# Optimization experiments

Hardware: AMD Instinct MI355X
Metric: run time of the kernel (lower is better)

The kernel has to match this reference:

```python
import jax, jax.numpy as jnp
import numpy as np

SIZES = [384, 160, 128, 96, 1]   # aev_length followed by hidden sizes (ANI-1 config)
N_SPECIES = 4                    # H, C, N, O
N_LAYERS = 4
CELU_ALPHA = 0.1
B, A = 128, 512                  # molecules, atoms per molecule


def setup_inputs() -> dict:
    key = jax.random.key(0)
    ks = jax.random.split(key, 2 + 2 * N_LAYERS)
    inp = {
        "fullaev": jax.random.normal(ks[0], (B, A, SIZES[0]), dtype=jnp.float32),
        "species": jax.random.randint(ks[1], (A,), 0, N_SPECIES, dtype=jnp.int32),
    }
    # Per-species stacked Linear params, torch default init: U(-1/sqrt(fan_in), 1/sqrt(fan_in))
    for l in range(N_LAYERS):
        bound = 1.0 / np.sqrt(SIZES[l])
        inp[f"W{l}"] = jax.random.uniform(ks[2 + 2 * l], (N_SPECIES, SIZES[l + 1], SIZES[l]),
                                          dtype=jnp.float32, minval=-bound, maxval=bound)
        inp[f"b{l}"] = jax.random.uniform(ks[3 + 2 * l], (N_SPECIES, SIZES[l + 1]),
                                          dtype=jnp.float32, minval=-bound, maxval=bound)
    return inp


def reference(fullaev, species, W0, b0, W1, b1, W2, b2, W3, b3):
    # fullaev: [B, A, aev_len]; species: [A] int route ids.
    # Equivalent to the per-atom Python loop: each atom goes through its
    # species' MLP; gather the per-atom weight matrices and do one batched GEMM per layer.
    Ws = (W0, W1, W2, W3)
    bs = (b0, b1, b2, b3)
    y = fullaev
    for l in range(N_LAYERS):
        Wa = Ws[l][species]          # [A, out, in] gathered per atom
        ba = bs[l][species]          # [A, out]
        y = jnp.einsum('bai,aoi->bao', y, Wa) + ba[None, :, :]
        if l < N_LAYERS - 1:
            y = jax.nn.celu(y, alpha=CELU_ALPHA)
    # stack over atoms + sum reducer over atom dim, then squeeze -> [B]
    return jnp.squeeze(jnp.sum(y, axis=1), axis=-1)
```

## Files before the change

kernel.cpp:

```cpp
#include <hip/hip_runtime.h>
#include <hip/hip_bf16.h>


typedef float f32x4 __attribute__((ext_vector_type(4)));
typedef short s16x8 __attribute__((ext_vector_type(8)));

#define NMOL   128
#define NATOM  512
#define AEV    384
#define MT     64
#define Y0LD   168
#define Y1LD   136
#define Y2LD   104

#define PL0    61440
#define PL1    20480
#define PL2    12288
#define BASE0  0
#define BASE1  245760
#define BASE2  327680
#define WP_BYTE_OFF 262144

typedef const __attribute__((address_space(1))) void* gas_ptr;
typedef __attribute__((address_space(3))) void* las_ptr;

__device__ __forceinline__ ushort f2bf(float f) {
    uint u = __float_as_uint(f);
    return (ushort)((u + 0x7fffu + ((u >> 16) & 1u)) >> 16);
}
__device__ __forceinline__ float bf2f(ushort h) {
    return __uint_as_float(((uint)h) << 16);
}
__device__ __forceinline__ float celu_f(float v) {
    return fmaxf(v, 0.0f) + fminf(0.1f * (__expf(10.0f * v) - 1.0f), 0.0f);
}
__device__ __forceinline__ uint pk2bf(float x, float y) {
    __hip_bfloat162 h2;
    h2.x = __float2bfloat16(x);
    h2.y = __float2bfloat16(y);
    return *(uint*)&h2;
}

__global__ __launch_bounds__(256) void prep_kernel(
    const float* __restrict__ W0, const float* __restrict__ W1,
    const float* __restrict__ W2, ushort* __restrict__ Wp)
{
    const int idx = blockIdx.x * 256 + threadIdx.x;
    int n, k0, KS;
    size_t base;
    const float* src;
    if (idx < 30720) {
        const int s = idx / 7680, r = idx % 7680;
        n = r / 48; k0 = (r % 48) * 8; KS = 12;
        src = W0 + (size_t)idx * 8;
        base = BASE0 + (size_t)s * PL0;
    } else if (idx < 40960) {
        const int i2 = idx - 30720;
        const int s = i2 / 2560, r = i2 % 2560;
        n = r / 20; k0 = (r % 20) * 8; KS = 5;
        src = W1 + (size_t)i2 * 8;
        base = BASE1 + (size_t)s * PL1;
    } else {
        const int i2 = idx - 40960;
        const int s = i2 / 1536, r = i2 % 1536;
        n = r / 16; k0 = (r % 16) * 8; KS = 4;
        src = W2 + (size_t)i2 * 8;
        base = BASE2 + (size_t)s * PL2;
    }
    const float4 v0 = *(const float4*)(src);
    const float4 v1 = *(const float4*)(src + 4);
    const size_t fo = (size_t)((((n >> 4) * KS + (k0 >> 5)) * 64
                                + ((k0 & 31) >> 3) * 16 + (n & 15)) * 8);
    uint4 w;
    w.x = (uint)f2bf(v0.x) | ((uint)f2bf(v0.y) << 16);
    w.y = (uint)f2bf(v0.z) | ((uint)f2bf(v0.w) << 16);
    w.z = (uint)f2bf(v1.x) | ((uint)f2bf(v1.y) << 16);
    w.w = (uint)f2bf(v1.z) | ((uint)f2bf(v1.w) << 16);
    *(uint4*)(Wp + base + fo) = w;
}

__global__ __attribute__((amdgpu_flat_work_group_size(512, 512),
                          amdgpu_waves_per_eu(8, 8)))
void ani_mfma_kernel(
    const float* __restrict__ aev, const int* __restrict__ species,
    const ushort* __restrict__ Wp,
    const float* __restrict__ b0, const float* __restrict__ b1,
    const float* __restrict__ b2,
    const float* __restrict__ W3, const float* __restrict__ b3,
    float* __restrict__ partial)
{
    __shared__ __align__(16) unsigned char smemA[17408];
    __shared__ __align__(16) unsigned char smemB[21504];

    const int bid  = blockIdx.x;
    const int a    = bid >> 1;
    const int half = bid & 1;
    const int tid  = threadIdx.x;
    const int lane = tid & 63;
    const int wid  = tid >> 6;
    const int mgrp = wid >> 2;
    const int ngrp = wid & 3;
    const bool has3 = (ngrp < 2);

    const int s = species[a];
    const ushort* Bh0 = Wp + BASE0 + (size_t)s * PL0;
    const ushort* Bh1 = Wp + BASE1 + (size_t)s * PL1;
    const ushort* Bh2 = Wp + BASE2 + (size_t)s * PL2;
    const float* b0s = b0 + s * 160;
    const float* b1s = b1 + s * 128;
    const float* b2s = b2 + s * 96;
    const float* w3s = W3 + s * 96;
    const float  bb3 = b3[s];

    ushort* y0buf = (ushort*)smemB;
    ushort* y1buf = (ushort*)smemA;

    const int mol8 = lane >> 3;
    const int swz  = (lane & 7) ^ mol8;
    const char* gsrc = (const char*)(aev
        + ((size_t)(half * MT + wid * 8 + mol8) * NATOM + a) * AEV) + swz * 16;
    const int ldsbase = wid * 1024;

    const f32x4 zero = {0.f, 0.f, 0.f, 0.f};
    f32x4 acc[2][3];
    #pragma unroll
    for (int mf = 0; mf < 2; ++mf)
        #pragma unroll
        for (int ti = 0; ti < 3; ++ti) acc[mf][ti] = zero;

    {
        const int r0 = mgrp * 32 + (lane & 15);
        const int c  = lane >> 4;

        __builtin_amdgcn_global_load_lds((gas_ptr)(gsrc),
                                         (las_ptr)(smemA + ldsbase), 16, 0, 0);
        __syncthreads();

        #pragma unroll
        for (int t = 0; t < 12; ++t) {
            if (t < 11)
                __builtin_amdgcn_global_load_lds(
                    (gas_ptr)(gsrc + (t + 1) * 128),
                    (las_ptr)(smemA + (((t + 1) & 1) * 8192) + ldsbase), 16, 0, 0);

            const float* Xb = (const float*)(smemA + (t & 1) * 8192);
            s16x8 ah[2];
            #pragma unroll
            for (int mf = 0; mf < 2; ++mf) {
                const int r = r0 + mf * 16;
                const float* rowp = Xb + r * 32;
                const f32x4 c0 = *(const f32x4*)(rowp + (((2 * c    ) ^ (r & 7)) * 4));
                const f32x4 c1 = *(const f32x4*)(rowp + (((2 * c + 1) ^ (r & 7)) * 4));
                union { s16x8 v; uint u[4]; } rr;
                rr.u[0] = pk2bf(c0.x, c0.y);
                rr.u[1] = pk2bf(c0.z, c0.w);
                rr.u[2] = pk2bf(c1.x, c1.y);
                rr.u[3] = pk2bf(c1.z, c1.w);
                ah[mf] = rr.v;
            }
            #pragma unroll
            for (int ti = 0; ti < 3; ++ti) {
                if (ti < 2 || has3) {
                    const s16x8 bh = *(const s16x8*)(
                        Bh0 + ((size_t)((ngrp + 4 * ti) * 12 + t) * 64 + lane) * 8);
                    acc[0][ti] = __builtin_amdgcn_mfma_f32_16x16x32_bf16(ah[0], bh, acc[0][ti], 0, 0, 0);
                    acc[1][ti] = __builtin_amdgcn_mfma_f32_16x16x32_bf16(ah[1], bh, acc[1][ti], 0, 0, 0);
                }
            }
            if (t < 11) __syncthreads();
        }
    }

    s16x8 b1r[2][5];
    #pragma unroll
    for (int ks = 0; ks < 5; ++ks) {
        b1r[0][ks] = *(const s16x8*)(Bh1 + ((size_t)((ngrp    ) * 5 + ks) * 64 + lane) * 8);
        b1r[1][ks] = *(const s16x8*)(Bh1 + ((size_t)((ngrp + 4) * 5 + ks) * 64 + lane) * 8);
    }

    #pragma unroll
    for (int ti = 0; ti < 3; ++ti) {
        if (ti < 2 || has3) {
            const int n = (ngrp + 4 * ti) * 16 + (lane & 15);
            const float bv = b0s[n];
            #pragma unroll
            for (int mf = 0; mf < 2; ++mf) {
                #pragma unroll
                for (int r = 0; r < 4; ++r) {
                    const int row = mgrp * 32 + mf * 16 + (lane >> 4) * 4 + r;
                    y0buf[row * Y0LD + n] = f2bf(celu_f(acc[mf][ti][r] + bv));
                }
            }
        }
    }
    __syncthreads();

    f32x4 acc1[2][2];
    #pragma unroll
    for (int mf = 0; mf < 2; ++mf) { acc1[mf][0] = zero; acc1[mf][1] = zero; }
    #pragma unroll
    for (int ks = 0; ks < 5; ++ks) {
        s16x8 ah[2];
        #pragma unroll
        for (int mf = 0; mf < 2; ++mf)
            ah[mf] = *(const s16x8*)(y0buf + (mgrp * 32 + mf * 16 + (lane & 15)) * Y0LD
                                     + ks * 32 + (lane >> 4) * 8);
        #pragma unroll
        for (int mf = 0; mf < 2; ++mf) {
            acc1[mf][0] = __builtin_amdgcn_mfma_f32_16x16x32_bf16(ah[mf], b1r[0][ks], acc1[mf][0], 0, 0, 0);
            acc1[mf][1] = __builtin_amdgcn_mfma_f32_16x16x32_bf16(ah[mf], b1r[1][ks], acc1[mf][1], 0, 0, 0);
        }
    }

    s16x8 b2r[2][4];
    #pragma unroll
    for (int ks = 0; ks < 4; ++ks)
        b2r[0][ks] = *(const s16x8*)(Bh2 + ((size_t)((ngrp) * 4 + ks) * 64 + lane) * 8);
    if (has3) {
        #pragma unroll
        for (int ks = 0; ks < 4; ++ks)
            b2r[1][ks] = *(const s16x8*)(Bh2 + ((size_t)((ngrp + 4) * 4 + ks) * 64 + lane) * 8);
    }

    #pragma unroll
    for (int t = 0; t < 2; ++t) {
        const int n = (ngrp + 4 * t) * 16 + (lane & 15);
        const float bv = b1s[n];
        #pragma unroll
        for (int mf = 0; mf < 2; ++mf) {
            #pragma unroll
            for (int r = 0; r < 4; ++r) {
                const int row = mgrp * 32 + mf * 16 + (lane >> 4) * 4 + r;
                y1buf[row * Y1LD + n] = f2bf(celu_f(acc1[mf][t][r] + bv));
            }
        }
    }
    __syncthreads();

    f32x4 acc2[2][2];
    #pragma unroll
    for (int mf = 0; mf < 2; ++mf) { acc2[mf][0] = zero; acc2[mf][1] = zero; }
    #pragma unroll
    for (int ks = 0; ks < 4; ++ks) {
        s16x8 ah[2];
        #pragma unroll
        for (int mf = 0; mf < 2; ++mf)
            ah[mf] = *(const s16x8*)(y1buf + (mgrp * 32 + mf * 16 + (lane & 15)) * Y1LD
                                     + ks * 32 + (lane >> 4) * 8);
        #pragma unroll
        for (int mf = 0; mf < 2; ++mf) {
            acc2[mf][0] = __builtin_amdgcn_mfma_f32_16x16x32_bf16(ah[mf], b2r[0][ks], acc2[mf][0], 0, 0, 0);
            if (has3)
                acc2[mf][1] = __builtin_amdgcn_mfma_f32_16x16x32_bf16(ah[mf], b2r[1][ks], acc2[mf][1], 0, 0, 0);
        }
    }
    __syncthreads();

    #pragma unroll
    for (int t = 0; t < 2; ++t) {
        if (t == 0 || has3) {
            const int n = (ngrp + 4 * t) * 16 + (lane & 15);
            const float bv = b2s[n];
            #pragma unroll
            for (int mf = 0; mf < 2; ++mf) {
                #pragma unroll
                for (int r = 0; r < 4; ++r) {
                    const int row = mgrp * 32 + mf * 16 + (lane >> 4) * 4 + r;
                    y0buf[row * Y2LD + n] = f2bf(celu_f(acc2[mf][t][r] + bv));
                }
            }
        }
    }
    __syncthreads();

    {
        float* red = (float*)smemA;
        const int m = tid & (MT - 1);
        const int q = tid >> 6;
        float accv = 0.f;
        #pragma unroll
        for (int ii = 0; ii < 12; ++ii) {
            const int i = q * 12 + ii;
            accv = fmaf(w3s[i], bf2f(y0buf[m * Y2LD + i]), accv);
        }
        red[q * MT + m] = accv;
        __syncthreads();
        if (tid < MT) {
            float sm = bb3;
            #pragma unroll
            for (int qq = 0; qq < 8; ++qq) sm += red[qq * MT + tid];
            partial[(size_t)a * NMOL + half * MT + tid] = sm;
        }
    }
}

__global__ __launch_bounds__(256) void reduce_kernel(
    const float* __restrict__ partial, float* __restrict__ out)
{
    __shared__ float red[256];
    const int m = blockIdx.x;
    const int t = threadIdx.x;
    float sv = partial[(size_t)t * NMOL + m] + partial[(size_t)(t + 256) * NMOL + m];
    red[t] = sv;
    __syncthreads();
    #pragma unroll
    for (int w = 128; w > 0; w >>= 1) {
        if (t < w) red[t] += red[t + w];
        __syncthreads();
    }
    if (t == 0) out[m] = red[0];
}

extern "C" void kernel_launch(void* const* d_in, const int* in_sizes, int n_in,
                              void* d_out, int out_size, void* d_ws, size_t ws_size,
                              hipStream_t stream) {
    const float* aev     = (const float*)d_in[0];
    const int*   species = (const int*)  d_in[1];
    const float* W0 = (const float*)d_in[2];
    const float* b0 = (const float*)d_in[3];
    const float* W1 = (const float*)d_in[4];
    const float* b1 = (const float*)d_in[5];
    const float* W2 = (const float*)d_in[6];
    const float* b2 = (const float*)d_in[7];
    const float* W3 = (const float*)d_in[8];
    const float* b3 = (const float*)d_in[9];
    float* out     = (float*)d_out;
    float* partial = (float*)d_ws;
    ushort* Wp     = (ushort*)((char*)d_ws + WP_BYTE_OFF);

    prep_kernel<<<184, 256, 0, stream>>>(W0, W1, W2, Wp);
    ani_mfma_kernel<<<NATOM * 2, 512, 0, stream>>>(aev, species, Wp,
                                                   b0, b1, b2, W3, b3, partial);
    reduce_kernel<<<NMOL, 256, 0, stream>>>(partial, out);
}
```

Measured before the change: 42.95 us.

## Triple-buffer layer-0 AEV tiles with prefetch distance two and hoisted weight loads

Grows the layer-0 LDS staging from double to triple buffering, so async global->LDS loads run two k-steps ahead, and waits with an explicit vmcnt plus a raw s_barrier. Weight fragment loads for each k-step are issued at the top of the iteration, ahead of the A-fragment conversion, to hide their latency. The occupancy hint drops from 8 to 6 waves per EU to fit the larger LDS use and more live registers. The vmcnt-based wait is fragile, since the hoisted weight loads also count toward vmcnt, which could let later steps read tiles that have not fully arrived.

```diff
diff --git a/kernel.cpp b/kernel.cpp
--- a/kernel.cpp
+++ b/kernel.cpp
@@ -80,7 +80,7 @@
 }
 
 __global__ __attribute__((amdgpu_flat_work_group_size(512, 512),
-                          amdgpu_waves_per_eu(8, 8)))
+                          amdgpu_waves_per_eu(6, 6)))
 void ani_mfma_kernel(
     const float* __restrict__ aev, const int* __restrict__ species,
     const ushort* __restrict__ Wp,
@@ -89,7 +89,7 @@
     const float* __restrict__ W3, const float* __restrict__ b3,
     float* __restrict__ partial)
 {
-    __shared__ __align__(16) unsigned char smemA[17408];
+    __shared__ __align__(16) unsigned char smemA[24576];
     __shared__ __align__(16) unsigned char smemB[21504];
 
     const int bid  = blockIdx.x;
@@ -134,16 +134,29 @@
 
         __builtin_amdgcn_global_load_lds((gas_ptr)(gsrc),
                                          (las_ptr)(smemA + ldsbase), 16, 0, 0);
-        __syncthreads();
+        __builtin_amdgcn_global_load_lds((gas_ptr)(gsrc + 128),
+                                         (las_ptr)(smemA + 8192 + ldsbase), 16, 0, 0);
+        asm volatile("s_waitcnt vmcnt(1)" ::: "memory");
+        __builtin_amdgcn_sched_barrier(0);
+        __builtin_amdgcn_s_barrier();
+        __builtin_amdgcn_sched_barrier(0);
 
         #pragma unroll
         for (int t = 0; t < 12; ++t) {
-            if (t < 11)
+            const s16x8 bh0 = *(const s16x8*)(
+                Bh0 + ((size_t)((ngrp    ) * 12 + t) * 64 + lane) * 8);
+            const s16x8 bh1 = *(const s16x8*)(
+                Bh0 + ((size_t)((ngrp + 4) * 12 + t) * 64 + lane) * 8);
+            s16x8 bh2;
+            if (has3) bh2 = *(const s16x8*)(
+                Bh0 + ((size_t)((ngrp + 8) * 12 + t) * 64 + lane) * 8);
+
+            if (t + 2 < 12)
                 __builtin_amdgcn_global_load_lds(
-                    (gas_ptr)(gsrc + (t + 1) * 128),
-                    (las_ptr)(smemA + (((t + 1) & 1) * 8192) + ldsbase), 16, 0, 0);
-
-            const float* Xb = (const float*)(smemA + (t & 1) * 8192);
+                    (gas_ptr)(gsrc + (t + 2) * 128),
+                    (las_ptr)(smemA + ((t + 2) % 3) * 8192 + ldsbase), 16, 0, 0);
+
+            const float* Xb = (const float*)(smemA + (t % 3) * 8192);
             s16x8 ah[2];
             #pragma unroll
             for (int mf = 0; mf < 2; ++mf) {
@@ -158,16 +171,19 @@
                 rr.u[3] = pk2bf(c1.z, c1.w);
                 ah[mf] = rr.v;
             }
-            #pragma unroll
-            for (int ti = 0; ti < 3; ++ti) {
-                if (ti < 2 || has3) {
-                    const s16x8 bh = *(const s16x8*)(
-                        Bh0 + ((size_t)((ngrp + 4 * ti) * 12 + t) * 64 + lane) * 8);
-                    acc[0][ti] = __builtin_amdgcn_mfma_f32_16x16x32_bf16(ah[0], bh, acc[0][ti], 0, 0, 0);
-                    acc[1][ti] = __builtin_amdgcn_mfma_f32_16x16x32_bf16(ah[1], bh, acc[1][ti], 0, 0, 0);
-                }
-            }
-            if (t < 11) __syncthreads();
+            acc[0][0] = __builtin_amdgcn_mfma_f32_16x16x32_bf16(ah[0], bh0, acc[0][0], 0, 0, 0);
+            acc[1][0] = __builtin_amdgcn_mfma_f32_16x16x32_bf16(ah[1], bh0, acc[1][0], 0, 0, 0);
+            acc[0][1] = __builtin_amdgcn_mfma_f32_16x16x32_bf16(ah[0], bh1, acc[0][1], 0, 0, 0);
+            acc[1][1] = __builtin_amdgcn_mfma_f32_16x16x32_bf16(ah[1], bh1, acc[1][1], 0, 0, 0);
+            if (has3) {
+                acc[0][2] = __builtin_amdgcn_mfma_f32_16x16x32_bf16(ah[0], bh2, acc[0][2], 0, 0, 0);
+                acc[1][2] = __builtin_amdgcn_mfma_f32_16x16x32_bf16(ah[1], bh2, acc[1][2], 0, 0, 0);
+            }
+            if (t < 11) {
+                __builtin_amdgcn_sched_barrier(0);
+                __builtin_amdgcn_s_barrier();
+                __builtin_amdgcn_sched_barrier(0);
+            }
         }
     }
 
@@ -222,6 +238,7 @@
             b2r[1][ks] = *(const s16x8*)(Bh2 + ((size_t)((ngrp + 4) * 4 + ks) * 64 + lane) * 8);
     }
 
+    ushort* Y1 = y1buf;
     #pragma unroll
     for (int t = 0; t < 2; ++t) {
         const int n = (ngrp + 4 * t) * 16 + (lane & 15);
@@ -231,7 +248,7 @@
             #pragma unroll
             for (int r = 0; r < 4; ++r) {
                 const int row = mgrp * 32 + mf * 16 + (lane >> 4) * 4 + r;
-                y1buf[row * Y1LD + n] = f2bf(celu_f(acc1[mf][t][r] + bv));
+                Y1[row * Y1LD + n] = f2bf(celu_f(acc1[mf][t][r] + bv));
             }
         }
     }
@@ -245,7 +262,7 @@
         s16x8 ah[2];
         #pragma unroll
         for (int mf = 0; mf < 2; ++mf)
-            ah[mf] = *(const s16x8*)(y1buf + (mgrp * 32 + mf * 16 + (lane & 15)) * Y1LD
+            ah[mf] = *(const s16x8*)(Y1 + (mgrp * 32 + mf * 16 + (lane & 15)) * Y1LD
                                      + ks * 32 + (lane >> 4) * 8);
         #pragma unroll
         for (int mf = 0; mf < 2; ++mf) {
```

Result: slower. 46.90 us (+9.2%).
